# Kernel tuning notes

Measured on AMD Instinct MI355X. Metric: run time of the kernel, lower is better.

The kernel has to match this reference:

```python
import jax, jax.numpy as jnp
import numpy as np

ATOM_FEA = 128
NBR_FEA = 64
NUM_NBR = 12
N_NODES = 50000
N_EDGES = N_NODES * NUM_NBR
BN_EPS = 1e-5


def setup_inputs() -> dict:
    key = jax.random.key(0)
    ks = jax.random.split(key, 8)
    x = jax.random.normal(ks[0], (N_NODES, ATOM_FEA), dtype=jnp.float32)
    # CGCNN layout: each node has exactly NUM_NBR edges, contiguous by source node
    src = jnp.repeat(jnp.arange(N_NODES, dtype=jnp.int64), NUM_NBR)
    nbr = jax.random.randint(ks[1], (N_EDGES,), 0, N_NODES, dtype=jnp.int64)
    edge_index = jnp.stack([src, nbr], axis=0)
    edge_attr = jax.random.normal(ks[2], (N_EDGES, NBR_FEA), dtype=jnp.float32)
    in_dim = 2 * ATOM_FEA + NBR_FEA
    out_dim = 2 * ATOM_FEA
    lim = 1.0 / np.sqrt(in_dim)
    W = jax.random.uniform(ks[3], (out_dim, in_dim), jnp.float32, -lim, lim)
    b = jax.random.uniform(ks[4], (out_dim,), jnp.float32, -lim, lim)
    bn1_g = jnp.ones((out_dim,), jnp.float32)
    bn1_b = jnp.zeros((out_dim,), jnp.float32)
    bn2_g = jnp.ones((ATOM_FEA,), jnp.float32)
    bn2_b = jnp.zeros((ATOM_FEA,), jnp.float32)
    return {"x": x, "edge_index": edge_index, "edge_attr": edge_attr,
            "W": W, "b": b, "bn1_g": bn1_g, "bn1_b": bn1_b,
            "bn2_g": bn2_g, "bn2_b": bn2_b}


def _batchnorm(h, gamma, beta):
    # training-mode BN: biased batch variance, eps=1e-5 (torch default)
    mean = jnp.mean(h, axis=0)
    var = jnp.var(h, axis=0)
    return (h - mean) * jax.lax.rsqrt(var + BN_EPS) * gamma + beta


def reference(x, edge_index, edge_attr, W, b, bn1_g, bn1_b, bn2_g, bn2_b):
    n_nodes, fea = x.shape
    num_nbr = edge_index.shape[1] // n_nodes
    # gather + concat: [E, 2F + nbr_fea]
    total = jnp.concatenate([x[edge_index[1]], x[edge_index[0]], edge_attr], axis=1)
    gated = total @ W.T + b                      # [E, 2F]
    gated = _batchnorm(gated, bn1_g, bn1_b)
    nbr_filter, nbr_core = jnp.split(gated, 2, axis=1)
    msg = jax.nn.sigmoid(nbr_filter) * jax.nn.softplus(nbr_core)  # [E, F]
    nbr_sumed = msg.reshape(n_nodes, num_nbr, fea).sum(axis=1)    # [N, F]
    nbr_sumed = _batchnorm(nbr_sumed, bn2_g, bn2_b)
    return jax.nn.softplus(x + nbr_sumed)
```

## Files before the change

kernel.cpp:

```cpp
#include <hip/hip_runtime.h>
#include <math.h>

#define ATOM_FEA 128
#define NBR_FEA  64
#define IN_DIM   320
#define OUT_DIM  256

#define M_TILE   48
#define GRID_G   768
#define GRID_3   1024
#define RB1      32

typedef float  f32x4 __attribute__((ext_vector_type(4)));
typedef short  s16x8 __attribute__((ext_vector_type(8)));

__device__ __forceinline__ float softplusf(float v) {
    float e = __expf(-fabsf(v));
    return fmaxf(v, 0.f) + __logf(1.f + e);
}
__device__ __forceinline__ float sigmoidf(float v) {
    return __builtin_amdgcn_rcpf(1.f + __expf(-v));
}
__device__ __forceinline__ unsigned short f2bf(float f) {
    unsigned u = __float_as_uint(f);
    return (unsigned short)((u + 0x7FFFu + ((u >> 16) & 1u)) >> 16);
}
__device__ __forceinline__ float bf2f(unsigned short h) {
    return __uint_as_float(((unsigned)h) << 16);
}
__device__ __forceinline__ unsigned pk2(float a, float b) {
    return (unsigned)f2bf(a) | ((unsigned)f2bf(b) << 16);
}

#define EA_OFF   0
#define EA_STR   144
#define X_OFF    6912
#define X_STR    520
#define SMEM2    31872

__global__ __launch_bounds__(256) void k1_mfma(
    const float* __restrict__ x, const float* __restrict__ W,
    unsigned short* __restrict__ Abf, unsigned short* __restrict__ Bbf,
    int nNodes)
{
    __shared__ alignas(16) char sx[64 * 272];
    const int tid  = threadIdx.x;
    const int wave = tid >> 6;
    const int lane = tid & 63;
    const int li   = lane & 15;
    const int quad = lane >> 4;
    const int cTile = blockIdx.x * 64;
    const int nTile = blockIdx.y * 64;
    const int cOff  = (cTile < 256) ? cTile : (cTile - 256);
    const int kBase = (cTile < 256) ? 0 : 128;
    unsigned short* dst = (cTile < 256) ? Abf : Bbf;

    s16x8 bf[4][4];
    #pragma unroll
    for (int ks = 0; ks < 4; ++ks)
        #pragma unroll
        for (int ns = 0; ns < 4; ++ns) {
            const float* wr = W + (size_t)(cOff + ns * 16 + li) * IN_DIM + kBase + ks * 32 + quad * 8;
            float4 va = *(const float4*)wr;
            float4 vb = *(const float4*)(wr + 4);
            union { uint4 u; s16x8 v; } cv;
            cv.u = make_uint4(pk2(va.x, va.y), pk2(va.z, va.w),
                              pk2(vb.x, vb.y), pk2(vb.z, vb.w));
            bf[ks][ns] = cv.v;
        }

    #pragma unroll
    for (int i = 0; i < 8; ++i) {
        int idx = tid + i * 256;
        int r = idx >> 5, q = idx & 31;
        int gn = nTile + r;
        float4 v = make_float4(0.f, 0.f, 0.f, 0.f);
        if (gn < nNodes) v = *(const float4*)(x + (size_t)gn * ATOM_FEA + q * 4);
        uint2 u; u.x = pk2(v.x, v.y); u.y = pk2(v.z, v.w);
        *(uint2*)(sx + r * 272 + q * 8) = u;
    }
    __syncthreads();

    s16x8 af[4];
    #pragma unroll
    for (int ks = 0; ks < 4; ++ks)
        af[ks] = *(const s16x8*)(sx + (wave * 16 + li) * 272 + (ks * 32 + quad * 8) * 2);

    f32x4 acc[4] = {};
    #pragma unroll
    for (int ks = 0; ks < 4; ++ks)
        #pragma unroll
        for (int ns = 0; ns < 4; ++ns)
            acc[ns] = __builtin_amdgcn_mfma_f32_16x16x32_bf16(af[ks], bf[ks][ns], acc[ns], 0, 0, 0);

    #pragma unroll
    for (int ns = 0; ns < 4; ++ns)
        #pragma unroll
        for (int r = 0; r < 4; ++r) {
            int node = nTile + wave * 16 + quad * 4 + r;
            if (node < nNodes)
                dst[(size_t)node * 256 + cOff + ns * 16 + li] = f2bf(acc[ns][r]);
        }
}

__global__ __launch_bounds__(256) void k2_fused(
    const unsigned short* __restrict__ Abf, const unsigned short* __restrict__ Bbf,
    const float* __restrict__ ea, const int* __restrict__ ei,
    const float* __restrict__ W, const float* __restrict__ bvec,
    unsigned short* __restrict__ gated, float* __restrict__ part,
    int nNodes, int nEdges)
{
    __shared__ alignas(16) char smem[SMEM2];
    const int tid  = threadIdx.x;
    const int wave = tid >> 6;
    const int lane = tid & 63;
    const int li   = lane & 15;
    const int quad = lane >> 4;

    s16x8 bfr[2][4];
    #pragma unroll
    for (int ks = 0; ks < 2; ++ks)
        #pragma unroll
        for (int ns = 0; ns < 4; ++ns) {
            int chn = wave * 64 + ns * 16 + li;
            const float* wr = W + (size_t)chn * IN_DIM + 256 + ks * 32 + quad * 8;
            float4 va = *(const float4*)wr;
            float4 vb = *(const float4*)(wr + 4);
            union { uint4 u; s16x8 v; } cv;
            cv.u = make_uint4(pk2(va.x, va.y), pk2(va.z, va.w),
                              pk2(vb.x, vb.y), pk2(vb.z, vb.w));
            bfr[ks][ns] = cv.v;
        }

    const int chq = lane;
    const float4 b4 = *(const float4*)(bvec + chq * 4);
    float4 s4  = {0.f, 0.f, 0.f, 0.f};
    float4 s24 = {0.f, 0.f, 0.f, 0.f};

    const int nTiles = (nEdges + M_TILE - 1) / M_TILE;
    for (int t = blockIdx.x; t < nTiles; t += gridDim.x) {
        const int tBase = t * M_TILE;
        #pragma unroll
        for (int i = 0; i < 3; ++i) {
            int idx = tid + i * 256;
            int r = idx >> 4, q = idx & 15;
            int ge = tBase + r;
            float4 v = make_float4(0.f, 0.f, 0.f, 0.f);
            if (ge < nEdges) v = *(const float4*)(ea + (size_t)ge * 64 + q * 4);
            uint2 u; u.x = pk2(v.x, v.y); u.y = pk2(v.z, v.w);
            *(uint2*)(smem + EA_OFF + r * EA_STR + q * 8) = u;
        }
        __syncthreads();

        s16x8 af[2][3];
        #pragma unroll
        for (int ks = 0; ks < 2; ++ks)
            #pragma unroll
            for (int ms = 0; ms < 3; ++ms)
                af[ks][ms] = *(const s16x8*)(smem + EA_OFF + (ms * 16 + li) * EA_STR + (ks * 32 + quad * 8) * 2);

        f32x4 acc[3][4] = {};
        #pragma unroll
        for (int ks = 0; ks < 2; ++ks)
            #pragma unroll
            for (int ms = 0; ms < 3; ++ms)
                #pragma unroll
                for (int ns = 0; ns < 4; ++ns)
                    acc[ms][ns] = __builtin_amdgcn_mfma_f32_16x16x32_bf16(
                        af[ks][ms], bfr[ks][ns], acc[ms][ns], 0, 0, 0);

        #pragma unroll
        for (int ms = 0; ms < 3; ++ms)
            #pragma unroll
            for (int ns = 0; ns < 4; ++ns) {
                int col = wave * 64 + ns * 16 + li;
                #pragma unroll
                for (int r = 0; r < 4; ++r) {
                    int row = ms * 16 + quad * 4 + r;
                    *(unsigned short*)(smem + X_OFF + row * X_STR + col * 2) = f2bf(acc[ms][ns][r]);
                }
            }
        __syncthreads();

        const int node = t * 4 + wave;
        if (node < nNodes) {
            uint2 bn2 = *(const uint2*)(Bbf + (size_t)node * 256 + chq * 4);
            const float Bn0 = bf2f((unsigned short)(bn2.x & 0xffffu));
            const float Bn1 = bf2f((unsigned short)(bn2.x >> 16));
            const float Bn2 = bf2f((unsigned short)(bn2.y & 0xffffu));
            const float Bn3 = bf2f((unsigned short)(bn2.y >> 16));
            const int e0 = tBase + wave * 12;
            #pragma unroll
            for (int j = 0; j < 12; ++j) {
                const int e = e0 + j;
                const int nb = ei[nEdges + e];
                uint2 a2 = *(const uint2*)(Abf + (size_t)nb * 256 + chq * 4);
                uint2 xv = *(const uint2*)(smem + X_OFF + (wave * 12 + j) * X_STR + chq * 8);
                float g0 = bf2f((unsigned short)(xv.x & 0xffffu)) + bf2f((unsigned short)(a2.x & 0xffffu)) + Bn0 + b4.x;
                float g1 = bf2f((unsigned short)(xv.x >> 16))     + bf2f((unsigned short)(a2.x >> 16))     + Bn1 + b4.y;
                float g2 = bf2f((unsigned short)(xv.y & 0xffffu)) + bf2f((unsigned short)(a2.y & 0xffffu)) + Bn2 + b4.z;
                float g3 = bf2f((unsigned short)(xv.y >> 16))     + bf2f((unsigned short)(a2.y >> 16))     + Bn3 + b4.w;
                s4.x += g0; s4.y += g1; s4.z += g2; s4.w += g3;
                s24.x = fmaf(g0, g0, s24.x); s24.y = fmaf(g1, g1, s24.y);
                s24.z = fmaf(g2, g2, s24.z); s24.w = fmaf(g3, g3, s24.w);
                uint2 o; o.x = pk2(g0, g1); o.y = pk2(g2, g3);
                *(uint2*)(gated + (size_t)e * 256 + chq * 4) = o;
            }
        }
    }

    __syncthreads();
    float* red = (float*)smem;
    *(float4*)(red + (size_t)(wave * 64 + chq) * 8)     = s4;
    *(float4*)(red + (size_t)(wave * 64 + chq) * 8 + 4) = s24;
    __syncthreads();
    {
        const int c = tid;
        const int g = c >> 2, k = c & 3;
        float s = 0.f, s2 = 0.f;
        #pragma unroll
        for (int w = 0; w < 4; ++w) {
            s  += red[(w * 64 + g) * 8 + k];
            s2 += red[(w * 64 + g) * 8 + 4 + k];
        }
        part[(size_t)blockIdx.x * 512 + c]       = s;
        part[(size_t)blockIdx.x * 512 + 256 + c] = s2;
    }
}

__global__ __launch_bounds__(512) void k2b1(
    const float* __restrict__ part, float* __restrict__ out, int nRows, int rowsPerBlk)
{
    const int c = threadIdx.x;
    int r0 = blockIdx.x * rowsPerBlk;
    int r1 = min(r0 + rowsPerBlk, nRows);
    float s = 0.f;
    for (int r = r0; r < r1; ++r) s += part[(size_t)r * 512 + c];
    out[(size_t)blockIdx.x * 512 + c] = s;
}
__global__ __launch_bounds__(256) void k2b2(
    const float* __restrict__ p1, const float* __restrict__ g1v,
    const float* __restrict__ b1v, float* __restrict__ stats, float invE)
{
    const int c = threadIdx.x;
    float s = 0.f, s2 = 0.f;
    for (int r = 0; r < RB1; ++r) {
        s  += p1[(size_t)r * 512 + c];
        s2 += p1[(size_t)r * 512 + 256 + c];
    }
    float mean = s * invE;
    float var = fmaf(-mean, mean, s2 * invE);
    float sc = g1v[c] * rsqrtf(var + 1e-5f);
    stats[c] = sc;
    stats[256 + c] = fmaf(-mean, sc, b1v[c]);
}

__global__ __launch_bounds__(256) void k3_msg2(
    const unsigned short* __restrict__ gated, const float* __restrict__ stats,
    float* __restrict__ NS, float* __restrict__ part2, int nNodes)
{
    const int tid = threadIdx.x;
    const int o  = tid & 15;
    const int nl = tid >> 4;
    float scF[8], shF[8], scC[8], shC[8];
    #pragma unroll
    for (int k = 0; k < 8; ++k) {
        int cf = o * 8 + k;
        scF[k] = stats[cf];        shF[k] = stats[256 + cf];
        scC[k] = stats[128 + cf];  shC[k] = stats[384 + cf];
    }
    float sA[8] = {}, s2A[8] = {};
    for (int n = blockIdx.x * 16 + nl; n < nNodes; n += gridDim.x * 16) {
        float m[8] = {};
        for (int j = 0; j < 12; ++j) {
            size_t base = (size_t)(n * 12 + j) * 256;
            uint4 uf = *(const uint4*)(gated + base + o * 8);
            uint4 uc = *(const uint4*)(gated + base + 128 + o * 8);
            unsigned fu[4] = {uf.x, uf.y, uf.z, uf.w};
            unsigned cu[4] = {uc.x, uc.y, uc.z, uc.w};
            #pragma unroll
            for (int q = 0; q < 4; ++q) {
                float f0 = fmaf(bf2f((unsigned short)(fu[q] & 0xffffu)), scF[q*2],   shF[q*2]);
                float f1 = fmaf(bf2f((unsigned short)(fu[q] >> 16)),     scF[q*2+1], shF[q*2+1]);
                float c0 = fmaf(bf2f((unsigned short)(cu[q] & 0xffffu)), scC[q*2],   shC[q*2]);
                float c1 = fmaf(bf2f((unsigned short)(cu[q] >> 16)),     scC[q*2+1], shC[q*2+1]);
                m[q*2]   = fmaf(sigmoidf(f0), softplusf(c0), m[q*2]);
                m[q*2+1] = fmaf(sigmoidf(f1), softplusf(c1), m[q*2+1]);
            }
        }
        float4 o0 = {m[0], m[1], m[2], m[3]};
        float4 o1 = {m[4], m[5], m[6], m[7]};
        *(float4*)(NS + (size_t)n * 128 + o * 8)     = o0;
        *(float4*)(NS + (size_t)n * 128 + o * 8 + 4) = o1;
        #pragma unroll
        for (int k = 0; k < 8; ++k) {
            sA[k] += m[k];
            s2A[k] = fmaf(m[k], m[k], s2A[k]);
        }
    }
    __shared__ float red[2][16][128];
    #pragma unroll
    for (int k = 0; k < 8; ++k) {
        red[0][nl][o * 8 + k] = sA[k];
        red[1][nl][o * 8 + k] = s2A[k];
    }
    __syncthreads();
    if (tid < 128) {
        float s = 0.f, s2 = 0.f;
        #pragma unroll
        for (int r = 0; r < 16; ++r) {
            s  += red[0][r][tid];
            s2 += red[1][r][tid];
        }
        part2[(size_t)blockIdx.x * 256 + tid]       = s;
        part2[(size_t)blockIdx.x * 256 + 128 + tid] = s2;
    }
}

__global__ __launch_bounds__(256) void k3b1(
    const float* __restrict__ part2, float* __restrict__ out, int nRows, int rowsPerBlk)
{
    const int c = threadIdx.x;
    int r0 = blockIdx.x * rowsPerBlk;
    int r1 = min(r0 + rowsPerBlk, nRows);
    float s = 0.f;
    for (int r = r0; r < r1; ++r) s += part2[(size_t)r * 256 + c];
    out[(size_t)blockIdx.x * 256 + c] = s;
}
__global__ __launch_bounds__(128) void k3b2(
    const float* __restrict__ p1, const float* __restrict__ g2v,
    const float* __restrict__ b2v, float* __restrict__ stats2, float invN)
{
    const int c = threadIdx.x;
    float s = 0.f, s2 = 0.f;
    for (int r = 0; r < RB1; ++r) {
        s  += p1[(size_t)r * 256 + c];
        s2 += p1[(size_t)r * 256 + 128 + c];
    }
    float mean = s * invN;
    float var = fmaf(-mean, mean, s2 * invN);
    float sc = g2v[c] * rsqrtf(var + 1e-5f);
    stats2[c] = sc;
    stats2[128 + c] = fmaf(-mean, sc, b2v[c]);
}

__global__ __launch_bounds__(256) void k4_final(
    const float* __restrict__ x, const float* __restrict__ ns,
    const float* __restrict__ stats2, float* __restrict__ out, int total4)
{
    int idx = blockIdx.x * 256 + threadIdx.x;
    for (int i = idx; i < total4; i += gridDim.x * 256) {
        int cq = i & 31;
        float4 xv = ((const float4*)x)[i];
        float4 sv = ((const float4*)ns)[i];
        float4 sc = ((const float4*)stats2)[cq];
        float4 sh = ((const float4*)(stats2 + 128))[cq];
        float4 o;
        o.x = softplusf(fmaf(sv.x, sc.x, sh.x) + xv.x);
        o.y = softplusf(fmaf(sv.y, sc.y, sh.y) + xv.y);
        o.z = softplusf(fmaf(sv.z, sc.z, sh.z) + xv.z);
        o.w = softplusf(fmaf(sv.w, sc.w, sh.w) + xv.w);
        ((float4*)out)[i] = o;
    }
}

extern "C" void kernel_launch(void* const* d_in, const int* in_sizes, int n_in,
                              void* d_out, int out_size, void* d_ws, size_t ws_size,
                              hipStream_t stream)
{
    const float* x   = (const float*)d_in[0];
    const int*   ei  = (const int*)d_in[1];
    const float* ea  = (const float*)d_in[2];
    const float* W   = (const float*)d_in[3];
    const float* b   = (const float*)d_in[4];
    const float* g1v = (const float*)d_in[5];
    const float* b1v = (const float*)d_in[6];
    const float* g2v = (const float*)d_in[7];
    const float* b2v = (const float*)d_in[8];
    float* out = (float*)d_out;

    const int nNodes = in_sizes[0] / ATOM_FEA;
    const int nEdges = in_sizes[1] / 2;

    unsigned short* Abf   = (unsigned short*)d_ws;
    unsigned short* Bbf   = Abf + (size_t)nNodes * 256;
    unsigned short* gated = Bbf + (size_t)nNodes * 256;
    float* NS  = (float*)(gated + (size_t)nEdges * 256);
    float* P1  = NS  + (size_t)nNodes * 128;
    float* P1b = P1  + (size_t)GRID_G * 512;
    float* P2  = P1b + (size_t)RB1 * 512;
    float* P2b = P2  + (size_t)GRID_3 * 256;
    float* S1  = P2b + (size_t)RB1 * 256;
    float* S2  = S1 + 512;
    (void)ws_size; (void)n_in; (void)out_size;

    dim3 grid1(8, (nNodes + 63) / 64);
    k1_mfma<<<grid1, 256, 0, stream>>>(x, W, Abf, Bbf, nNodes);

    k2_fused<<<GRID_G, 256, 0, stream>>>(Abf, Bbf, ea, ei, W, b, gated, P1, nNodes, nEdges);
    k2b1<<<RB1, 512, 0, stream>>>(P1, P1b, GRID_G, (GRID_G + RB1 - 1) / RB1);
    k2b2<<<1, 256, 0, stream>>>(P1b, g1v, b1v, S1, 1.f / (float)nEdges);
    k3_msg2<<<GRID_3, 256, 0, stream>>>(gated, S1, NS, P2, nNodes);
    k3b1<<<RB1, 256, 0, stream>>>(P2, P2b, GRID_3, (GRID_3 + RB1 - 1) / RB1);
    k3b2<<<1, 128, 0, stream>>>(P2b, g2v, b2v, S2, 1.f / (float)nNodes);
    k4_final<<<2048, 256, 0, stream>>>(x, NS, S2, out, nNodes * 32);
}
```

Measured before the change: 657.7 us.

## Drop LDS staging in edge kernel by swapping MFMA operands for direct register epilogue

The edge kernel no longer stages edge attributes and MFMA outputs through shared memory. Each lane loads its own edge row from global memory and converts it to bf16 with a hardware packed-convert instruction. Swapping the MFMA operands transposes the accumulator layout, so each lane holds four contiguous channels of one edge and can add the gathered neighbour and self terms and store directly. The bias is folded into the precomputed self term in the first kernel, and the per-block BN statistics are reduced with cross-lane shuffles instead of LDS, which removes both barriers per tile. In exchange, each lane issues more scattered small global loads for the neighbour and self rows.

```diff
diff --git a/kernel.cpp b/kernel.cpp
--- a/kernel.cpp
+++ b/kernel.cpp
@@ -21,25 +21,18 @@
 __device__ __forceinline__ float sigmoidf(float v) {
     return __builtin_amdgcn_rcpf(1.f + __expf(-v));
 }
-__device__ __forceinline__ unsigned short f2bf(float f) {
-    unsigned u = __float_as_uint(f);
-    return (unsigned short)((u + 0x7FFFu + ((u >> 16) & 1u)) >> 16);
-}
 __device__ __forceinline__ float bf2f(unsigned short h) {
     return __uint_as_float(((unsigned)h) << 16);
 }
 __device__ __forceinline__ unsigned pk2(float a, float b) {
-    return (unsigned)f2bf(a) | ((unsigned)f2bf(b) << 16);
-}
-
-#define EA_OFF   0
-#define EA_STR   144
-#define X_OFF    6912
-#define X_STR    520
-#define SMEM2    31872
+    unsigned r;
+    asm("v_cvt_pk_bf16_f32 %0, %1, %2" : "=v"(r) : "v"(a), "v"(b));
+    return r;
+}
 
 __global__ __launch_bounds__(256) void k1_mfma(
     const float* __restrict__ x, const float* __restrict__ W,
+    const float* __restrict__ bvec,
     unsigned short* __restrict__ Abf, unsigned short* __restrict__ Bbf,
     int nNodes)
 {
@@ -91,26 +84,30 @@
     for (int ks = 0; ks < 4; ++ks)
         #pragma unroll
         for (int ns = 0; ns < 4; ++ns)
-            acc[ns] = __builtin_amdgcn_mfma_f32_16x16x32_bf16(af[ks], bf[ks][ns], acc[ns], 0, 0, 0);
-
-    #pragma unroll
-    for (int ns = 0; ns < 4; ++ns)
-        #pragma unroll
-        for (int r = 0; r < 4; ++r) {
-            int node = nTile + wave * 16 + quad * 4 + r;
-            if (node < nNodes)
-                dst[(size_t)node * 256 + cOff + ns * 16 + li] = f2bf(acc[ns][r]);
-        }
+            acc[ns] = __builtin_amdgcn_mfma_f32_16x16x32_bf16(bf[ks][ns], af[ks], acc[ns], 0, 0, 0);
+
+    const int node = nTile + wave * 16 + li;
+    if (node < nNodes) {
+        #pragma unroll
+        for (int ns = 0; ns < 4; ++ns) {
+            const int c0 = cOff + ns * 16 + quad * 4;
+            float4 bb = make_float4(0.f, 0.f, 0.f, 0.f);
+            if (kBase) bb = *(const float4*)(bvec + c0);
+            uint2 o;
+            o.x = pk2(acc[ns][0] + bb.x, acc[ns][1] + bb.y);
+            o.y = pk2(acc[ns][2] + bb.z, acc[ns][3] + bb.w);
+            *(uint2*)(dst + (size_t)node * 256 + c0) = o;
+        }
+    }
 }
 
 __global__ __launch_bounds__(256) void k2_fused(
     const unsigned short* __restrict__ Abf, const unsigned short* __restrict__ Bbf,
     const float* __restrict__ ea, const int* __restrict__ ei,
-    const float* __restrict__ W, const float* __restrict__ bvec,
+    const float* __restrict__ W,
     unsigned short* __restrict__ gated, float* __restrict__ part,
-    int nNodes, int nEdges)
-{
-    __shared__ alignas(16) char smem[SMEM2];
+    int nEdges)
+{
     const int tid  = threadIdx.x;
     const int wave = tid >> 6;
     const int lane = tid & 63;
@@ -132,99 +129,108 @@
             bfr[ks][ns] = cv.v;
         }
 
-    const int chq = lane;
-    const float4 b4 = *(const float4*)(bvec + chq * 4);
-    float4 s4  = {0.f, 0.f, 0.f, 0.f};
-    float4 s24 = {0.f, 0.f, 0.f, 0.f};
+    int noff[3];
+    #pragma unroll
+    for (int ms = 0; ms < 3; ++ms) noff[ms] = (int)((unsigned)(ms * 16 + li) / 12u);
+
+    const int cB = wave * 64 + quad * 4;
+
+    f32x4 s4[4]  = {};
+    f32x4 s24[4] = {};
 
     const int nTiles = (nEdges + M_TILE - 1) / M_TILE;
     for (int t = blockIdx.x; t < nTiles; t += gridDim.x) {
         const int tBase = t * M_TILE;
-        #pragma unroll
-        for (int i = 0; i < 3; ++i) {
-            int idx = tid + i * 256;
-            int r = idx >> 4, q = idx & 15;
-            int ge = tBase + r;
-            float4 v = make_float4(0.f, 0.f, 0.f, 0.f);
-            if (ge < nEdges) v = *(const float4*)(ea + (size_t)ge * 64 + q * 4);
-            uint2 u; u.x = pk2(v.x, v.y); u.y = pk2(v.z, v.w);
-            *(uint2*)(smem + EA_OFF + r * EA_STR + q * 8) = u;
-        }
-        __syncthreads();
-
-        s16x8 af[2][3];
-        #pragma unroll
-        for (int ks = 0; ks < 2; ++ks)
+
+        int nb[3];
+        #pragma unroll
+        for (int ms = 0; ms < 3; ++ms) {
+            int e = tBase + ms * 16 + li;
+            nb[ms] = (e < nEdges) ? ei[nEdges + e] : 0;
+        }
+
+        #pragma unroll
+        for (int ms = 0; ms < 3; ++ms) {
+            const int e    = tBase + ms * 16 + li;
+            const bool ok  = (e < nEdges);
+            const int node = t * 4 + noff[ms];
+
+            uint2 a2[4], b2[4];
+            if (ok) {
+                #pragma unroll
+                for (int ns = 0; ns < 4; ++ns) {
+                    const int c0 = cB + ns * 16;
+                    a2[ns] = *(const uint2*)(Abf + (size_t)nb[ms] * 256 + c0);
+                    b2[ns] = *(const uint2*)(Bbf + (size_t)node * 256 + c0);
+                }
+            }
+
+            s16x8 af[2];
             #pragma unroll
-            for (int ms = 0; ms < 3; ++ms)
-                af[ks][ms] = *(const s16x8*)(smem + EA_OFF + (ms * 16 + li) * EA_STR + (ks * 32 + quad * 8) * 2);
-
-        f32x4 acc[3][4] = {};
-        #pragma unroll
-        for (int ks = 0; ks < 2; ++ks)
+            for (int ks = 0; ks < 2; ++ks) {
+                float4 va = make_float4(0.f, 0.f, 0.f, 0.f);
+                float4 vb = make_float4(0.f, 0.f, 0.f, 0.f);
+                if (ok) {
+                    const float* er = ea + (size_t)e * NBR_FEA + ks * 32 + quad * 8;
+                    va = *(const float4*)er;
+                    vb = *(const float4*)(er + 4);
+                }
+                union { uint4 u; s16x8 v; } cv;
+                cv.u = make_uint4(pk2(va.x, va.y), pk2(va.z, va.w),
+                                  pk2(vb.x, vb.y), pk2(vb.z, vb.w));
+                af[ks] = cv.v;
+            }
+
+            f32x4 acc[4] = {};
             #pragma unroll
-            for (int ms = 0; ms < 3; ++ms)
+            for (int ks = 0; ks < 2; ++ks)
                 #pragma unroll
                 for (int ns = 0; ns < 4; ++ns)
-                    acc[ms][ns] = __builtin_amdgcn_mfma_f32_16x16x32_bf16(
-                        af[ks][ms], bfr[ks][ns], acc[ms][ns], 0, 0, 0);
-
-        #pragma unroll
-        for (int ms = 0; ms < 3; ++ms)
-            #pragma unroll
-            for (int ns = 0; ns < 4; ++ns) {
-                int col = wave * 64 + ns * 16 + li;
+                    acc[ns] = __builtin_amdgcn_mfma_f32_16x16x32_bf16(
+                        bfr[ks][ns], af[ks], acc[ns], 0, 0, 0);
+
+            if (ok) {
                 #pragma unroll
-                for (int r = 0; r < 4; ++r) {
-                    int row = ms * 16 + quad * 4 + r;
-                    *(unsigned short*)(smem + X_OFF + row * X_STR + col * 2) = f2bf(acc[ms][ns][r]);
+                for (int ns = 0; ns < 4; ++ns) {
+                    const int c0 = cB + ns * 16;
+                    float g0 = acc[ns][0] + bf2f((unsigned short)(a2[ns].x & 0xffffu))
+                                          + bf2f((unsigned short)(b2[ns].x & 0xffffu));
+                    float g1 = acc[ns][1] + bf2f((unsigned short)(a2[ns].x >> 16))
+                                          + bf2f((unsigned short)(b2[ns].x >> 16));
+                    float g2 = acc[ns][2] + bf2f((unsigned short)(a2[ns].y & 0xffffu))
+                                          + bf2f((unsigned short)(b2[ns].y & 0xffffu));
+                    float g3 = acc[ns][3] + bf2f((unsigned short)(a2[ns].y >> 16))
+                                          + bf2f((unsigned short)(b2[ns].y >> 16));
+                    s4[ns][0] += g0; s4[ns][1] += g1; s4[ns][2] += g2; s4[ns][3] += g3;
+                    s24[ns][0] = fmaf(g0, g0, s24[ns][0]);
+                    s24[ns][1] = fmaf(g1, g1, s24[ns][1]);
+                    s24[ns][2] = fmaf(g2, g2, s24[ns][2]);
+                    s24[ns][3] = fmaf(g3, g3, s24[ns][3]);
+                    uint2 o; o.x = pk2(g0, g1); o.y = pk2(g2, g3);
+                    *(uint2*)(gated + (size_t)e * 256 + c0) = o;
                 }
             }
-        __syncthreads();
-
-        const int node = t * 4 + wave;
-        if (node < nNodes) {
-            uint2 bn2 = *(const uint2*)(Bbf + (size_t)node * 256 + chq * 4);
-            const float Bn0 = bf2f((unsigned short)(bn2.x & 0xffffu));
-            const float Bn1 = bf2f((unsigned short)(bn2.x >> 16));
-            const float Bn2 = bf2f((unsigned short)(bn2.y & 0xffffu));
-            const float Bn3 = bf2f((unsigned short)(bn2.y >> 16));
-            const int e0 = tBase + wave * 12;
+        }
+    }
+
+    #pragma unroll
+    for (int m = 1; m < 16; m <<= 1) {
+        #pragma unroll
+        for (int ns = 0; ns < 4; ++ns) {
             #pragma unroll
-            for (int j = 0; j < 12; ++j) {
-                const int e = e0 + j;
-                const int nb = ei[nEdges + e];
-                uint2 a2 = *(const uint2*)(Abf + (size_t)nb * 256 + chq * 4);
-                uint2 xv = *(const uint2*)(smem + X_OFF + (wave * 12 + j) * X_STR + chq * 8);
-                float g0 = bf2f((unsigned short)(xv.x & 0xffffu)) + bf2f((unsigned short)(a2.x & 0xffffu)) + Bn0 + b4.x;
-                float g1 = bf2f((unsigned short)(xv.x >> 16))     + bf2f((unsigned short)(a2.x >> 16))     + Bn1 + b4.y;
-                float g2 = bf2f((unsigned short)(xv.y & 0xffffu)) + bf2f((unsigned short)(a2.y & 0xffffu)) + Bn2 + b4.z;
-                float g3 = bf2f((unsigned short)(xv.y >> 16))     + bf2f((unsigned short)(a2.y >> 16))     + Bn3 + b4.w;
-                s4.x += g0; s4.y += g1; s4.z += g2; s4.w += g3;
-                s24.x = fmaf(g0, g0, s24.x); s24.y = fmaf(g1, g1, s24.y);
-                s24.z = fmaf(g2, g2, s24.z); s24.w = fmaf(g3, g3, s24.w);
-                uint2 o; o.x = pk2(g0, g1); o.y = pk2(g2, g3);
-                *(uint2*)(gated + (size_t)e * 256 + chq * 4) = o;
+            for (int k = 0; k < 4; ++k) {
+                s4[ns][k]  += __shfl_xor(s4[ns][k],  m);
+                s24[ns][k] += __shfl_xor(s24[ns][k], m);
             }
         }
     }
-
-    __syncthreads();
-    float* red = (float*)smem;
-    *(float4*)(red + (size_t)(wave * 64 + chq) * 8)     = s4;
-    *(float4*)(red + (size_t)(wave * 64 + chq) * 8 + 4) = s24;
-    __syncthreads();
-    {
-        const int c = tid;
-        const int g = c >> 2, k = c & 3;
-        float s = 0.f, s2 = 0.f;
-        #pragma unroll
-        for (int w = 0; w < 4; ++w) {
-            s  += red[(w * 64 + g) * 8 + k];
-            s2 += red[(w * 64 + g) * 8 + 4 + k];
-        }
-        part[(size_t)blockIdx.x * 512 + c]       = s;
-        part[(size_t)blockIdx.x * 512 + 256 + c] = s2;
+    if (li == 0) {
+        #pragma unroll
+        for (int ns = 0; ns < 4; ++ns) {
+            const int c0 = cB + ns * 16;
+            *(f32x4*)(part + (size_t)blockIdx.x * 512 + c0)       = s4[ns];
+            *(f32x4*)(part + (size_t)blockIdx.x * 512 + 256 + c0) = s24[ns];
+        }
     }
 }
 
@@ -395,9 +401,9 @@
     (void)ws_size; (void)n_in; (void)out_size;
 
     dim3 grid1(8, (nNodes + 63) / 64);
-    k1_mfma<<<grid1, 256, 0, stream>>>(x, W, Abf, Bbf, nNodes);
-
-    k2_fused<<<GRID_G, 256, 0, stream>>>(Abf, Bbf, ea, ei, W, b, gated, P1, nNodes, nEdges);
+    k1_mfma<<<grid1, 256, 0, stream>>>(x, W, b, Abf, Bbf, nNodes);
+
+    k2_fused<<<GRID_G, 256, 0, stream>>>(Abf, Bbf, ea, ei, W, gated, P1, nEdges);
     k2b1<<<RB1, 512, 0, stream>>>(P1, P1b, GRID_G, (GRID_G + RB1 - 1) / RB1);
     k2b2<<<1, 256, 0, stream>>>(P1b, g1v, b1v, S1, 1.f / (float)nEdges);
     k3_msg2<<<GRID_3, 256, 0, stream>>>(gated, S1, NS, P2, nNodes);
```

New measurement: 691.4 us. +5.1%, slower.
